# Optimization experiments

Hardware: AMD Instinct MI355X
Metric: run time of the kernel (lower is better)

## Reference

```python
import jax, jax.numpy as jnp
import numpy as np
from jax import lax

B, T, N, CIN, CH, COUT, K, KS, E = 2, 16, 2048, 32, 64, 64, 3, 3, 32768


def setup_inputs() -> dict:
    key = jax.random.key(0)
    ks = jax.random.split(key, 20)
    s = 0.05
    p = lambda k, shp: s * jax.random.normal(k, shp, dtype=jnp.float32)
    return {
        "X": jax.random.normal(ks[0], (B, T, N, CIN), dtype=jnp.float32),
        "edge_index": jax.random.randint(ks[1], (2, E), 0, N),
        "edge_weight": jax.random.uniform(ks[2], (E,), dtype=jnp.float32),
        "tc1_w1": p(ks[3], (CH, CIN, 1, KS)), "tc1_b1": p(ks[4], (CH,)),
        "tc1_w2": p(ks[5], (CH, CIN, 1, KS)), "tc1_b2": p(ks[6], (CH,)),
        "tc1_w3": p(ks[7], (CH, CIN, 1, KS)), "tc1_b3": p(ks[8], (CH,)),
        "cheb_w": p(ks[9], (K, CH, CH)), "cheb_b": p(ks[10], (CH,)),
        "tc2_w1": p(ks[11], (COUT, CH, 1, KS)), "tc2_b1": p(ks[12], (COUT,)),
        "tc2_w2": p(ks[13], (COUT, CH, 1, KS)), "tc2_b2": p(ks[14], (COUT,)),
        "tc2_w3": p(ks[15], (COUT, CH, 1, KS)), "tc2_b3": p(ks[16], (COUT,)),
        "bn_gamma": jnp.ones((N,), jnp.float32),
        "bn_beta": jnp.zeros((N,), jnp.float32),
    }


def _tconv(X, w1, b1, w2, b2, w3, b3):
    # X: (B, T, N, C) -> (B, C, N, T), gated temporal conv over last axis
    x = jnp.transpose(X, (0, 3, 2, 1))
    dn = ("NCHW", "OIHW", "NCHW")
    c = lambda w, b: lax.conv_general_dilated(x, w, (1, 1), "VALID", dimension_numbers=dn) + b[None, :, None, None]
    out = jax.nn.relu(c(w1, b1) + jax.nn.sigmoid(c(w2, b2)) + c(w3, b3))
    return jnp.transpose(out, (0, 3, 2, 1))


def _cheb(x, edge_index, edge_weight, W, b):
    # ChebConv, sym normalization, lambda_max=2 -> L_hat = -D^{-1/2} A D^{-1/2}
    row, col = edge_index[0], edge_index[1]
    w = jnp.where(row == col, 0.0, edge_weight)  # get_laplacian removes self-loops
    deg = jax.ops.segment_sum(w, row, num_segments=N)
    safe = jnp.where(deg > 0, deg, 1.0)
    dis = jnp.where(deg > 0, lax.rsqrt(safe), 0.0)
    norm = -dis[row] * w * dis[col]  # (E,)

    def prop(z):  # z: (B, T, N, C)
        zm = jnp.moveaxis(z, 2, 0)                      # (N, B, T, C)
        msg = zm[col] * norm[:, None, None, None]       # (E, B, T, C)
        agg = jax.ops.segment_sum(msg, row, num_segments=N)
        return jnp.moveaxis(agg, 0, 2)

    Tx0 = x
    out = jnp.einsum("btnc,co->btno", Tx0, W[0])
    Tx1 = prop(Tx0)
    out = out + jnp.einsum("btnc,co->btno", Tx1, W[1])
    for k in range(2, K):
        Tx2 = 2.0 * prop(Tx1) - Tx0
        out = out + jnp.einsum("btnc,co->btno", Tx2, W[k])
        Tx0, Tx1 = Tx1, Tx2
    return out + b


def reference(X, edge_index, edge_weight, tc1_w1, tc1_b1, tc1_w2, tc1_b2, tc1_w3, tc1_b3,
              cheb_w, cheb_b, tc2_w1, tc2_b1, tc2_w2, tc2_b2, tc2_w3, tc2_b3,
              bn_gamma, bn_beta):
    t1 = _tconv(X, tc1_w1, tc1_b1, tc1_w2, tc1_b2, tc1_w3, tc1_b3)   # (B, T-2, N, CH)
    t2 = jax.nn.relu(_cheb(t1, edge_index, edge_weight, cheb_w, cheb_b))
    t3 = _tconv(t2, tc2_w1, tc2_b1, tc2_w2, tc2_b2, tc2_w3, tc2_b3)  # (B, T-4, N, COUT)
    t = jnp.transpose(t3, (0, 2, 1, 3))  # (B, N, T', COUT): N is BN channel axis
    mu = jnp.mean(t, axis=(0, 2, 3), keepdims=True)
    var = jnp.var(t, axis=(0, 2, 3), keepdims=True)
    t = (t - mu) * lax.rsqrt(var + 1e-5) * bn_gamma[None, :, None, None] + bn_beta[None, :, None, None]
    return jnp.transpose(t, (0, 2, 1, 3))
```

## Files before the change

### kernel.cpp

```cpp
#include <hip/hip_runtime.h>
#include <cstdint>
#include <cstddef>

typedef unsigned short ushort_t;
typedef short bf16x8 __attribute__((ext_vector_type(8)));
typedef unsigned short u16x8 __attribute__((ext_vector_type(8)));
typedef float f32x4 __attribute__((ext_vector_type(4)));

#define N_NODES 2048
#define E_EDGES 32768
#define BKT_CAP 64

constexpr int SMALL_TOTAL = 72128;
constexpr int OFS_T1B1 = 6144;
constexpr int OFS_T1B2 = 12352;
constexpr int OFS_T1B3 = 18560;
constexpr int OFS_CHB  = 30912;
constexpr int OFS_T2B1 = 43264;
constexpr int OFS_T2B2 = 55616;
constexpr int OFS_T2B3 = 67968;
constexpr int OFS_GAM  = 68032;
constexpr int OFS_BET  = 70080;

__device__ __align__(16) ushort_t g_t1b [3670016];
__device__ __align__(16) ushort_t g_tx1b[3670016];
__device__ __align__(16) ushort_t g_t2b [3670016];
__device__ __align__(16) float    g_t3 [3145728];
__device__ float    g_deg[N_NODES];
__device__ int      g_cnt[N_NODES];
__device__ int      g_cur[N_NODES];
__device__ __align__(8) int2 g_bkt[N_NODES * BKT_CAP];
__device__ __align__(16) ushort_t g_can[SMALL_TOTAL];
__device__ __align__(16) ushort_t g_wb1[18432];
__device__ __align__(16) ushort_t g_wb2[36864];
__device__ __align__(16) ushort_t g_wbc[12288];

__device__ __forceinline__ float bfu(ushort_t u) { return __uint_as_float(((unsigned)u) << 16); }
__device__ __forceinline__ ushort_t f2bf(float f) {
    unsigned u = __float_as_uint(f);
    u = u + 0x7fffu + ((u >> 16) & 1u);
    return (ushort_t)(u >> 16);
}
__device__ __forceinline__ float ldin(const void* p, int i, bool isbf) {
    return isbf ? bfu(((const ushort_t*)p)[i]) : ((const float*)p)[i];
}
#define BF16_ONES_PAIR 0x3F803F80u

struct SmallPtrs { const void* p[16]; };
struct WPtrs { const void* p[7]; };

__global__ __launch_bounds__(256) void setup_kernel(const int* __restrict__ ei,
                                                    const void* __restrict__ ew,
                                                    SmallPtrs sp, WPtrs wp,
                                                    const unsigned* __restrict__ gam) {
    const bool isbf = (gam[0] == BF16_ONES_PAIR);
    const int blk = blockIdx.x;
    const int tid = threadIdx.x;
    if (blk < 128) {
        int e = blk * 256 + tid;
        int r = ei[e];
        int c = ei[E_EDGES + e];
        float w = (r == c) ? 0.f : ldin(ew, e, isbf);
        atomicAdd(&g_deg[r], w);
        atomicAdd(&g_cnt[r], 1);
        return;
    }
    if (blk < 410) {
        const int sizes[16] = {6144, 64, 6144, 64, 6144, 64, 12288, 64,
                               12288, 64, 12288, 64, 12288, 64, 2048, 2048};
        int idx = (blk - 128) * 256 + tid;
        if (idx >= SMALL_TOTAL) return;
        int j = 0, local = idx;
        while (local >= sizes[j]) { local -= sizes[j]; ++j; }
        g_can[idx] = isbf ? ((const ushort_t*)sp.p[j])[local]
                          : f2bf(((const float*)sp.p[j])[local]);
        return;
    }
    int idx = (blk - 410) * 256 + tid;
    if (idx < 18432) {
        int j = idx & 7, lane = (idx >> 3) & 63, kk = (idx >> 9) % 3;
        int nt = (idx / 1536) & 3, set = idx / 6144;
        int o = nt * 16 + (lane & 15);
        int k = kk * 32 + (lane >> 4) * 8 + j;
        int ci = k & 31, ks = k >> 5;
        g_wb1[idx] = f2bf(ldin(wp.p[set], o * 96 + ci * 3 + ks, isbf));
    } else if (idx < 18432 + 36864) {
        int t = idx - 18432;
        int j = t & 7, lane = (t >> 3) & 63, kk = (t >> 9) % 6;
        int nt = (t / 3072) & 3, set = t / 12288;
        int o = nt * 16 + (lane & 15);
        int k = kk * 32 + (lane >> 4) * 8 + j;
        int ci = k & 63, ks = k >> 6;
        g_wb2[t] = f2bf(ldin(wp.p[3 + set], o * 192 + ci * 3 + ks, isbf));
    } else {
        int t = idx - 18432 - 36864;
        int j = t & 7, lane = (t >> 3) & 63, kk = (t >> 9) % 6;
        int nt = t / 3072;
        int o = nt * 16 + (lane & 15);
        int k = kk * 32 + (lane >> 4) * 8 + j;
        int sec = k >> 6, c = k & 63;
        g_wbc[t] = f2bf(ldin(wp.p[6], sec * 4096 + c * 64 + o, isbf));
    }
}

template <int LAYER>
__global__ __launch_bounds__(256) void tconv_mfma_kernel(const void* __restrict__ Xraw,
                                                         const int* __restrict__ ei,
                                                         const void* __restrict__ ew,
                                                         const unsigned* __restrict__ gam) {
    constexpr int T_in  = (LAYER == 1) ? 16 : 14;
    constexpr int T_out = (LAYER == 1) ? 14 : 12;
    constexpr int KST   = (LAYER == 1) ? 3 : 6;
    constexpr int PADK  = (LAYER == 1) ? 104 : 200;
    constexpr int OB1 = (LAYER == 1) ? OFS_T1B1 : OFS_T2B1;
    constexpr int OB2 = (LAYER == 1) ? OFS_T1B2 : OFS_T2B2;
    constexpr int OB3 = (LAYER == 1) ? OFS_T1B3 : OFS_T2B3;

    const bool isbf = (gam[0] == BF16_ONES_PAIR);

    if constexpr (LAYER == 1) {
        if (blockIdx.x >= 896) {
            int e = (blockIdx.x - 896) * 256 + threadIdx.x;
            int r = ei[e];
            int c = ei[E_EDGES + e];
            float w = (r == c) ? 0.f : ldin(ew, e, isbf);
            float dr = g_deg[r], dc = g_deg[c];
            float nr = dr > 0.f ? rsqrtf(dr) : 0.f;
            float nc = dc > 0.f ? rsqrtf(dc) : 0.f;
            int pos = atomicAdd(&g_cur[r], 1);
            g_bkt[(r << 6) + pos] = make_int2(c, __float_as_int(-nr * w * nc));
            return;
        }
    }

    __shared__ __align__(16) ushort_t xs[64 * PADK];

    const int tid = threadIdx.x;
    const int lane = tid & 63;
    const int wv = tid >> 6;
    const int m0 = blockIdx.x * 64;
    const int n0 = m0 & (N_NODES - 1);
    const int s  = m0 >> 11;
    const int b  = s / T_out;
    const int t  = s - b * T_out;

#pragma unroll
    for (int ks = 0; ks < 3; ++ks) {
        if constexpr (LAYER == 1) {
            const size_t elo = ((size_t)(b * T_in + t + ks) * N_NODES + n0) * 32;
            if (isbf) {
                const ushort4* src = (const ushort4*)((const ushort_t*)Xraw + elo);
                for (int i = tid; i < 512; i += 256) {
                    ushort4 v = src[i];
                    int row = i >> 3, c4 = i & 7;
                    *(ushort4*)&xs[row * PADK + ks * 32 + c4 * 4] = v;
                }
            } else {
                const float4* src = (const float4*)((const float*)Xraw + elo);
                for (int i = tid; i < 512; i += 256) {
                    float4 f = src[i];
                    ushort4 v;
                    v.x = f2bf(f.x); v.y = f2bf(f.y); v.z = f2bf(f.z); v.w = f2bf(f.w);
                    int row = i >> 3, c4 = i & 7;
                    *(ushort4*)&xs[row * PADK + ks * 32 + c4 * 4] = v;
                }
            }
        } else {
            const ushort4* src = (const ushort4*)(g_t2b +
                ((size_t)(b * T_in + t + ks) * N_NODES + n0) * 64);
            for (int i = tid; i < 1024; i += 256) {
                ushort4 v = src[i];
                int row = i >> 4, c4 = i & 15;
                *(ushort4*)&xs[row * PADK + ks * 64 + c4 * 4] = v;
            }
        }
    }
    __syncthreads();

    const ushort_t* WB = (LAYER == 1) ? g_wb1 : g_wb2;
    f32x4 acc[3][4];
#pragma unroll
    for (int st = 0; st < 3; ++st)
#pragma unroll
        for (int nt = 0; nt < 4; ++nt) acc[st][nt] = (f32x4){0.f, 0.f, 0.f, 0.f};

    const int arow = wv * 16 + (lane & 15);
    const int kofs = (lane >> 4) * 8;
#pragma unroll
    for (int kk = 0; kk < KST; ++kk) {
        bf16x8 av = *(const bf16x8*)&xs[arow * PADK + kk * 32 + kofs];
#pragma unroll
        for (int st = 0; st < 3; ++st)
#pragma unroll
            for (int nt = 0; nt < 4; ++nt) {
                bf16x8 bv = ((const bf16x8*)WB)[((st * 4 + nt) * KST + kk) * 64 + lane];
                acc[st][nt] = __builtin_amdgcn_mfma_f32_16x16x32_bf16(av, bv, acc[st][nt], 0, 0, 0);
            }
    }

    const int col = lane & 15;
    const int quad = lane >> 4;
#pragma unroll
    for (int nt = 0; nt < 4; ++nt) {
        int o = nt * 16 + col;
        float b1 = bfu(g_can[OB1 + o]);
        float b2 = bfu(g_can[OB2 + o]);
        float b3 = bfu(g_can[OB3 + o]);
#pragma unroll
        for (int reg = 0; reg < 4; ++reg) {
            int m = m0 + wv * 16 + quad * 4 + reg;
            float q = acc[1][nt][reg] + b2;
            float v = (acc[0][nt][reg] + b1) + 1.f / (1.f + expf(-q)) + (acc[2][nt][reg] + b3);
            v = v > 0.f ? v : 0.f;
            if constexpr (LAYER == 1) g_t1b[(size_t)m * 64 + o] = f2bf(v);
            else                      g_t3 [(size_t)m * 64 + o] = v;
        }
    }
}

__global__ __launch_bounds__(256) void prop0_kernel() {
    const int n = blockIdx.x;
    const int tid = threadIdx.x;
    const int slice = tid >> 3;
    const int ch8   = (tid & 7) * 8;
    if (slice >= 28) return;

    const int beg = n << 6;
    const int end = beg + g_cnt[n];
    const size_t soff = (size_t)slice * (N_NODES * 64) + ch8;

    float a[8];
#pragma unroll
    for (int k = 0; k < 8; ++k) a[k] = 0.f;

    int e = beg;
    for (; e + 4 <= end; e += 4) {
        int2 p0 = g_bkt[e];
        int2 p1 = g_bkt[e + 1];
        int2 p2 = g_bkt[e + 2];
        int2 p3 = g_bkt[e + 3];
        float w0 = __int_as_float(p0.y);
        float w1 = __int_as_float(p1.y);
        float w2 = __int_as_float(p2.y);
        float w3 = __int_as_float(p3.y);
        u16x8 v0 = *(const u16x8*)&g_t1b[soff + ((size_t)p0.x << 6)];
        u16x8 v1 = *(const u16x8*)&g_t1b[soff + ((size_t)p1.x << 6)];
        u16x8 v2 = *(const u16x8*)&g_t1b[soff + ((size_t)p2.x << 6)];
        u16x8 v3 = *(const u16x8*)&g_t1b[soff + ((size_t)p3.x << 6)];
#pragma unroll
        for (int k = 0; k < 8; ++k)
            a[k] = fmaf(w0, bfu(v0[k]), fmaf(w1, bfu(v1[k]),
                   fmaf(w2, bfu(v2[k]), fmaf(w3, bfu(v3[k]), a[k]))));
    }
    for (; e < end; ++e) {
        int2 p = g_bkt[e];
        float w = __int_as_float(p.y);
        u16x8 v = *(const u16x8*)&g_t1b[soff + ((size_t)p.x << 6)];
#pragma unroll
        for (int k = 0; k < 8; ++k) a[k] = fmaf(w, bfu(v[k]), a[k]);
    }

    const size_t o = soff + ((size_t)n << 6);
    u16x8 r;
#pragma unroll
    for (int k = 0; k < 8; ++k) r[k] = f2bf(a[k]);
    *(u16x8*)&g_tx1b[o] = r;
}

__global__ __launch_bounds__(256) void prop_cheb_kernel() {
    __shared__ __align__(16) ushort_t xs[32 * 200];

    const int n = blockIdx.x;
    const int tid = threadIdx.x;
    const int slice = tid >> 3;
    const int ch8   = (tid & 7) * 8;

    if (slice < 28) {
        const int beg = n << 6;
        const int end = beg + g_cnt[n];
        const size_t soff = (size_t)slice * (N_NODES * 64) + ch8;

        float a[8];
#pragma unroll
        for (int k = 0; k < 8; ++k) a[k] = 0.f;

        int e = beg;
        for (; e + 4 <= end; e += 4) {
            int2 p0 = g_bkt[e];
            int2 p1 = g_bkt[e + 1];
            int2 p2 = g_bkt[e + 2];
            int2 p3 = g_bkt[e + 3];
            float w0 = __int_as_float(p0.y);
            float w1 = __int_as_float(p1.y);
            float w2 = __int_as_float(p2.y);
            float w3 = __int_as_float(p3.y);
            u16x8 v0 = *(const u16x8*)&g_tx1b[soff + ((size_t)p0.x << 6)];
            u16x8 v1 = *(const u16x8*)&g_tx1b[soff + ((size_t)p1.x << 6)];
            u16x8 v2 = *(const u16x8*)&g_tx1b[soff + ((size_t)p2.x << 6)];
            u16x8 v3 = *(const u16x8*)&g_tx1b[soff + ((size_t)p3.x << 6)];
#pragma unroll
            for (int k = 0; k < 8; ++k)
                a[k] = fmaf(w0, bfu(v0[k]), fmaf(w1, bfu(v1[k]),
                       fmaf(w2, bfu(v2[k]), fmaf(w3, bfu(v3[k]), a[k]))));
        }
        for (; e < end; ++e) {
            int2 p = g_bkt[e];
            float w = __int_as_float(p.y);
            u16x8 v = *(const u16x8*)&g_tx1b[soff + ((size_t)p.x << 6)];
#pragma unroll
            for (int k = 0; k < 8; ++k) a[k] = fmaf(w, bfu(v[k]), a[k]);
        }

        const size_t o = soff + ((size_t)n << 6);
        u16x8 t0 = *(const u16x8*)&g_t1b[o];
        u16x8 t1 = *(const u16x8*)&g_tx1b[o];
        u16x8 t2;
#pragma unroll
        for (int k = 0; k < 8; ++k) t2[k] = f2bf(2.f * a[k] - bfu(t0[k]));

        *(u16x8*)&xs[slice * 200 + ch8]        = t0;
        *(u16x8*)&xs[slice * 200 + 64 + ch8]   = t1;
        *(u16x8*)&xs[slice * 200 + 128 + ch8]  = t2;
    } else {
        int r = 28 + ((tid - 224) >> 3);
        u16x8 z = {0, 0, 0, 0, 0, 0, 0, 0};
        *(u16x8*)&xs[r * 200 + ch8]       = z;
        *(u16x8*)&xs[r * 200 + 64 + ch8]  = z;
        *(u16x8*)&xs[r * 200 + 128 + ch8] = z;
    }
    __syncthreads();

    const int lane = tid & 63;
    const int wv = tid >> 6;
    const int mt = wv >> 1;
    const int ntb = (wv & 1) * 2;
    const int arow = mt * 16 + (lane & 15);
    const int kofs = (lane >> 4) * 8;

    f32x4 acc[2];
    acc[0] = (f32x4){0.f, 0.f, 0.f, 0.f};
    acc[1] = (f32x4){0.f, 0.f, 0.f, 0.f};
#pragma unroll
    for (int kk = 0; kk < 6; ++kk) {
        bf16x8 av = *(const bf16x8*)&xs[arow * 200 + kk * 32 + kofs];
#pragma unroll
        for (int i = 0; i < 2; ++i) {
            bf16x8 bv = ((const bf16x8*)g_wbc)[((ntb + i) * 6 + kk) * 64 + lane];
            acc[i] = __builtin_amdgcn_mfma_f32_16x16x32_bf16(av, bv, acc[i], 0, 0, 0);
        }
    }

    const int col = lane & 15;
    const int quad = lane >> 4;
#pragma unroll
    for (int i = 0; i < 2; ++i) {
        int o = (ntb + i) * 16 + col;
        float bias = bfu(g_can[OFS_CHB + o]);
#pragma unroll
        for (int reg = 0; reg < 4; ++reg) {
            int m = mt * 16 + quad * 4 + reg;
            if (m < 28) {
                float v = acc[i][reg] + bias;
                g_t2b[((size_t)(m * N_NODES + n)) * 64 + o] = f2bf(v > 0.f ? v : 0.f);
            }
        }
    }
}

__global__ __launch_bounds__(256) void bn_fused_kernel(void* __restrict__ outp,
                                                       const unsigned* __restrict__ gam) {
    int n = blockIdx.x;
    int tid = threadIdx.x;

    if (n < 8) {
        int z = n * 256 + tid;
        g_deg[z] = 0.f; g_cnt[z] = 0; g_cur[z] = 0;
    }

    int q = tid & 15;
    int g = tid >> 4;
    const bool two = (g < 8);

    size_t base0 = ((size_t)(g * N_NODES + n)) * 64 + q * 4;
    float4 v0 = *reinterpret_cast<const float4*>(&g_t3[base0]);
    float s1 = v0.x + v0.y + v0.z + v0.w;
    float s2 = v0.x * v0.x + v0.y * v0.y + v0.z * v0.z + v0.w * v0.w;
    size_t base1 = 0;
    float4 v1 = make_float4(0.f, 0.f, 0.f, 0.f);
    if (two) {
        base1 = ((size_t)((g + 16) * N_NODES + n)) * 64 + q * 4;
        v1 = *reinterpret_cast<const float4*>(&g_t3[base1]);
        s1 += v1.x + v1.y + v1.z + v1.w;
        s2 += v1.x * v1.x + v1.y * v1.y + v1.z * v1.z + v1.w * v1.w;
    }

    __shared__ float r1[256], r2[256];
    __shared__ float sc_s, sh_s;
    r1[tid] = s1;
    r2[tid] = s2;
    __syncthreads();
    for (int st = 128; st > 0; st >>= 1) {
        if (tid < st) { r1[tid] += r1[tid + st]; r2[tid] += r2[tid + st]; }
        __syncthreads();
    }
    if (tid == 0) {
        const float inv = 1.f / 1536.f;
        float mean = r1[0] * inv;
        float var  = r2[0] * inv - mean * mean;
        float rstd = rsqrtf(var + 1e-5f);
        float gm = bfu(g_can[OFS_GAM + n]), be = bfu(g_can[OFS_BET + n]);
        sc_s = rstd * gm;
        sh_s = be - mean * rstd * gm;
    }
    __syncthreads();
    float sc = sc_s, sh = sh_s;
    bool isbf = (gam[0] == BF16_ONES_PAIR);

    if (isbf) {
        ushort4 o0;
        o0.x = f2bf(v0.x * sc + sh); o0.y = f2bf(v0.y * sc + sh);
        o0.z = f2bf(v0.z * sc + sh); o0.w = f2bf(v0.w * sc + sh);
        *reinterpret_cast<ushort4*>((ushort_t*)outp + base0) = o0;
        if (two) {
            ushort4 o1;
            o1.x = f2bf(v1.x * sc + sh); o1.y = f2bf(v1.y * sc + sh);
            o1.z = f2bf(v1.z * sc + sh); o1.w = f2bf(v1.w * sc + sh);
            *reinterpret_cast<ushort4*>((ushort_t*)outp + base1) = o1;
        }
    } else {
        float4 o0 = make_float4(v0.x * sc + sh, v0.y * sc + sh, v0.z * sc + sh, v0.w * sc + sh);
        *reinterpret_cast<float4*>((float*)outp + base0) = o0;
        if (two) {
            float4 o1 = make_float4(v1.x * sc + sh, v1.y * sc + sh, v1.z * sc + sh, v1.w * sc + sh);
            *reinterpret_cast<float4*>((float*)outp + base1) = o1;
        }
    }
}

extern "C" void kernel_launch(void* const* d_in, const int* in_sizes, int n_in,
                              void* d_out, int out_size, void* d_ws, size_t ws_size,
                              hipStream_t stream) {
    const void* X = d_in[0];
    const int* ei = (const int*)d_in[1];
    const void* ew = d_in[2];
    const unsigned* gam = (const unsigned*)d_in[17];

    SmallPtrs sp;
    for (int i = 0; i < 16; ++i) sp.p[i] = d_in[3 + i];
    WPtrs wp;
    wp.p[0] = d_in[3];  wp.p[1] = d_in[5];  wp.p[2] = d_in[7];
    wp.p[3] = d_in[11]; wp.p[4] = d_in[13]; wp.p[5] = d_in[15];
    wp.p[6] = d_in[9];

    setup_kernel<<<674, 256, 0, stream>>>(ei, ew, sp, wp, gam);
    tconv_mfma_kernel<1><<<1024, 256, 0, stream>>>(X, ei, ew, gam);
    prop0_kernel<<<N_NODES, 256, 0, stream>>>();
    prop_cheb_kernel<<<N_NODES, 256, 0, stream>>>();
    tconv_mfma_kernel<2><<<768, 256, 0, stream>>>(X, nullptr, nullptr, gam);
    bn_fused_kernel<<<N_NODES, 256, 0, stream>>>(d_out, gam);
}
```

Measured before the change: 164.9 us.

## Fuse Chebyshev projection, second temporal conv and batchnorm into one per-node kernel

Merges the cheb output projection, the second gated temporal convolution and the per-node batch norm into one kernel with one block per node. The relu'd cheb output stays in shared memory and feeds the tconv2 MFMA directly, and the batch-norm statistics are reduced from registers. This removes the g_t2b and g_t3 global round trips and two kernel launches. In exchange the per-node blocks do small MFMA tiles with padded rows, and the scratch-counter reset moves to the end of the fused kernel.

```diff
diff --git a/kernel.cpp b/kernel.cpp
--- a/kernel.cpp
+++ b/kernel.cpp
@@ -24,8 +24,6 @@
 
 __device__ __align__(16) ushort_t g_t1b [3670016];
 __device__ __align__(16) ushort_t g_tx1b[3670016];
-__device__ __align__(16) ushort_t g_t2b [3670016];
-__device__ __align__(16) float    g_t3 [3145728];
 __device__ float    g_deg[N_NODES];
 __device__ int      g_cnt[N_NODES];
 __device__ int      g_cur[N_NODES];
@@ -103,34 +101,28 @@
     }
 }
 
-template <int LAYER>
-__global__ __launch_bounds__(256) void tconv_mfma_kernel(const void* __restrict__ Xraw,
-                                                         const int* __restrict__ ei,
-                                                         const void* __restrict__ ew,
-                                                         const unsigned* __restrict__ gam) {
-    constexpr int T_in  = (LAYER == 1) ? 16 : 14;
-    constexpr int T_out = (LAYER == 1) ? 14 : 12;
-    constexpr int KST   = (LAYER == 1) ? 3 : 6;
-    constexpr int PADK  = (LAYER == 1) ? 104 : 200;
-    constexpr int OB1 = (LAYER == 1) ? OFS_T1B1 : OFS_T2B1;
-    constexpr int OB2 = (LAYER == 1) ? OFS_T1B2 : OFS_T2B2;
-    constexpr int OB3 = (LAYER == 1) ? OFS_T1B3 : OFS_T2B3;
+__global__ __launch_bounds__(256) void tconv1_mfma_kernel(const void* __restrict__ Xraw,
+                                                          const int* __restrict__ ei,
+                                                          const void* __restrict__ ew,
+                                                          const unsigned* __restrict__ gam) {
+    constexpr int T_in  = 16;
+    constexpr int T_out = 14;
+    constexpr int KST   = 3;
+    constexpr int PADK  = 104;
 
     const bool isbf = (gam[0] == BF16_ONES_PAIR);
 
-    if constexpr (LAYER == 1) {
-        if (blockIdx.x >= 896) {
-            int e = (blockIdx.x - 896) * 256 + threadIdx.x;
-            int r = ei[e];
-            int c = ei[E_EDGES + e];
-            float w = (r == c) ? 0.f : ldin(ew, e, isbf);
-            float dr = g_deg[r], dc = g_deg[c];
-            float nr = dr > 0.f ? rsqrtf(dr) : 0.f;
-            float nc = dc > 0.f ? rsqrtf(dc) : 0.f;
-            int pos = atomicAdd(&g_cur[r], 1);
-            g_bkt[(r << 6) + pos] = make_int2(c, __float_as_int(-nr * w * nc));
-            return;
-        }
+    if (blockIdx.x >= 896) {
+        int e = (blockIdx.x - 896) * 256 + threadIdx.x;
+        int r = ei[e];
+        int c = ei[E_EDGES + e];
+        float w = (r == c) ? 0.f : ldin(ew, e, isbf);
+        float dr = g_deg[r], dc = g_deg[c];
+        float nr = dr > 0.f ? rsqrtf(dr) : 0.f;
+        float nc = dc > 0.f ? rsqrtf(dc) : 0.f;
+        int pos = atomicAdd(&g_cur[r], 1);
+        g_bkt[(r << 6) + pos] = make_int2(c, __float_as_int(-nr * w * nc));
+        return;
     }
 
     __shared__ __align__(16) ushort_t xs[64 * PADK];
@@ -146,38 +138,27 @@
 
 #pragma unroll
     for (int ks = 0; ks < 3; ++ks) {
-        if constexpr (LAYER == 1) {
-            const size_t elo = ((size_t)(b * T_in + t + ks) * N_NODES + n0) * 32;
-            if (isbf) {
-                const ushort4* src = (const ushort4*)((const ushort_t*)Xraw + elo);
-                for (int i = tid; i < 512; i += 256) {
-                    ushort4 v = src[i];
-                    int row = i >> 3, c4 = i & 7;
-                    *(ushort4*)&xs[row * PADK + ks * 32 + c4 * 4] = v;
-                }
-            } else {
-                const float4* src = (const float4*)((const float*)Xraw + elo);
-                for (int i = tid; i < 512; i += 256) {
-                    float4 f = src[i];
-                    ushort4 v;
-                    v.x = f2bf(f.x); v.y = f2bf(f.y); v.z = f2bf(f.z); v.w = f2bf(f.w);
-                    int row = i >> 3, c4 = i & 7;
-                    *(ushort4*)&xs[row * PADK + ks * 32 + c4 * 4] = v;
-                }
+        const size_t elo = ((size_t)(b * T_in + t + ks) * N_NODES + n0) * 32;
+        if (isbf) {
+            const ushort4* src = (const ushort4*)((const ushort_t*)Xraw + elo);
+            for (int i = tid; i < 512; i += 256) {
+                ushort4 v = src[i];
+                int row = i >> 3, c4 = i & 7;
+                *(ushort4*)&xs[row * PADK + ks * 32 + c4 * 4] = v;
             }
         } else {
-            const ushort4* src = (const ushort4*)(g_t2b +
-                ((size_t)(b * T_in + t + ks) * N_NODES + n0) * 64);
-            for (int i = tid; i < 1024; i += 256) {
-                ushort4 v = src[i];
-                int row = i >> 4, c4 = i & 15;
-                *(ushort4*)&xs[row * PADK + ks * 64 + c4 * 4] = v;
+            const float4* src = (const float4*)((const float*)Xraw + elo);
+            for (int i = tid; i < 512; i += 256) {
+                float4 f = src[i];
+                ushort4 v;
+                v.x = f2bf(f.x); v.y = f2bf(f.y); v.z = f2bf(f.z); v.w = f2bf(f.w);
+                int row = i >> 3, c4 = i & 7;
+                *(ushort4*)&xs[row * PADK + ks * 32 + c4 * 4] = v;
             }
         }
     }
     __syncthreads();
 
-    const ushort_t* WB = (LAYER == 1) ? g_wb1 : g_wb2;
     f32x4 acc[3][4];
 #pragma unroll
     for (int st = 0; st < 3; ++st)
@@ -193,7 +174,7 @@
         for (int st = 0; st < 3; ++st)
 #pragma unroll
             for (int nt = 0; nt < 4; ++nt) {
-                bf16x8 bv = ((const bf16x8*)WB)[((st * 4 + nt) * KST + kk) * 64 + lane];
+                bf16x8 bv = ((const bf16x8*)g_wb1)[((st * 4 + nt) * KST + kk) * 64 + lane];
                 acc[st][nt] = __builtin_amdgcn_mfma_f32_16x16x32_bf16(av, bv, acc[st][nt], 0, 0, 0);
             }
     }
@@ -203,17 +184,16 @@
 #pragma unroll
     for (int nt = 0; nt < 4; ++nt) {
         int o = nt * 16 + col;
-        float b1 = bfu(g_can[OB1 + o]);
-        float b2 = bfu(g_can[OB2 + o]);
-        float b3 = bfu(g_can[OB3 + o]);
+        float b1 = bfu(g_can[OFS_T1B1 + o]);
+        float b2 = bfu(g_can[OFS_T1B2 + o]);
+        float b3 = bfu(g_can[OFS_T1B3 + o]);
 #pragma unroll
         for (int reg = 0; reg < 4; ++reg) {
             int m = m0 + wv * 16 + quad * 4 + reg;
             float q = acc[1][nt][reg] + b2;
             float v = (acc[0][nt][reg] + b1) + 1.f / (1.f + expf(-q)) + (acc[2][nt][reg] + b3);
             v = v > 0.f ? v : 0.f;
-            if constexpr (LAYER == 1) g_t1b[(size_t)m * 64 + o] = f2bf(v);
-            else                      g_t3 [(size_t)m * 64 + o] = v;
+            g_t1b[(size_t)m * 64 + o] = f2bf(v);
         }
     }
 }
@@ -267,8 +247,12 @@
     *(u16x8*)&g_tx1b[o] = r;
 }
 
-__global__ __launch_bounds__(256) void prop_cheb_kernel() {
+__global__ __launch_bounds__(256) void fused_tail_kernel(void* __restrict__ outp,
+                                                         const unsigned* __restrict__ gam) {
     __shared__ __align__(16) ushort_t xs[32 * 200];
+    __shared__ __align__(16) ushort_t t2s[28 * 72];
+    __shared__ float r1[256], r2[256];
+    __shared__ float sc_s, sh_s;
 
     const int n = blockIdx.x;
     const int tid = threadIdx.x;
@@ -334,68 +318,83 @@
     const int wv = tid >> 6;
     const int mt = wv >> 1;
     const int ntb = (wv & 1) * 2;
-    const int arow = mt * 16 + (lane & 15);
-    const int kofs = (lane >> 4) * 8;
-
-    f32x4 acc[2];
-    acc[0] = (f32x4){0.f, 0.f, 0.f, 0.f};
-    acc[1] = (f32x4){0.f, 0.f, 0.f, 0.f};
-#pragma unroll
-    for (int kk = 0; kk < 6; ++kk) {
-        bf16x8 av = *(const bf16x8*)&xs[arow * 200 + kk * 32 + kofs];
-#pragma unroll
-        for (int i = 0; i < 2; ++i) {
-            bf16x8 bv = ((const bf16x8*)g_wbc)[((ntb + i) * 6 + kk) * 64 + lane];
-            acc[i] = __builtin_amdgcn_mfma_f32_16x16x32_bf16(av, bv, acc[i], 0, 0, 0);
-        }
-    }
-
     const int col = lane & 15;
     const int quad = lane >> 4;
+    const int arow = mt * 16 + col;
+    const int kofs = quad * 8;
+
+    {
+        f32x4 accb[2];
+        accb[0] = (f32x4){0.f, 0.f, 0.f, 0.f};
+        accb[1] = (f32x4){0.f, 0.f, 0.f, 0.f};
+#pragma unroll
+        for (int kk = 0; kk < 6; ++kk) {
+            bf16x8 av = *(const bf16x8*)&xs[arow * 200 + kk * 32 + kofs];
+#pragma unroll
+            for (int i = 0; i < 2; ++i) {
+                bf16x8 bv = ((const bf16x8*)g_wbc)[((ntb + i) * 6 + kk) * 64 + lane];
+                accb[i] = __builtin_amdgcn_mfma_f32_16x16x32_bf16(av, bv, accb[i], 0, 0, 0);
+            }
+        }
+#pragma unroll
+        for (int i = 0; i < 2; ++i) {
+            int o = (ntb + i) * 16 + col;
+            float bias = bfu(g_can[OFS_CHB + o]);
+#pragma unroll
+            for (int reg = 0; reg < 4; ++reg) {
+                int s = mt * 16 + quad * 4 + reg;
+                if (s < 28) {
+                    float v = accb[i][reg] + bias;
+                    t2s[s * 72 + o] = f2bf(v > 0.f ? v : 0.f);
+                }
+            }
+        }
+    }
+    __syncthreads();
+
+    const int m_a = arow;
+    const int bb  = (m_a >= 12) ? 1 : 0;
+    const int rbase = (m_a < 24) ? (m_a + 2 * bb) : 0;
+
+    f32x4 acc2[3][2];
+#pragma unroll
+    for (int st = 0; st < 3; ++st)
+#pragma unroll
+        for (int i = 0; i < 2; ++i) acc2[st][i] = (f32x4){0.f, 0.f, 0.f, 0.f};
+
+#pragma unroll
+    for (int kk = 0; kk < 6; ++kk) {
+        const int ks = kk >> 1;
+        const int ci0 = (kk & 1) * 32;
+        bf16x8 av = *(const bf16x8*)&t2s[(rbase + ks) * 72 + ci0 + kofs];
+#pragma unroll
+        for (int st = 0; st < 3; ++st)
+#pragma unroll
+            for (int i = 0; i < 2; ++i) {
+                bf16x8 bv = ((const bf16x8*)g_wb2)[((st * 4 + ntb + i) * 6 + kk) * 64 + lane];
+                acc2[st][i] = __builtin_amdgcn_mfma_f32_16x16x32_bf16(av, bv, acc2[st][i], 0, 0, 0);
+            }
+    }
+
+    float y[2][4];
+    float s1 = 0.f, s2 = 0.f;
 #pragma unroll
     for (int i = 0; i < 2; ++i) {
         int o = (ntb + i) * 16 + col;
-        float bias = bfu(g_can[OFS_CHB + o]);
+        float b1 = bfu(g_can[OFS_T2B1 + o]);
+        float b2 = bfu(g_can[OFS_T2B2 + o]);
+        float b3 = bfu(g_can[OFS_T2B3 + o]);
 #pragma unroll
         for (int reg = 0; reg < 4; ++reg) {
-            int m = mt * 16 + quad * 4 + reg;
-            if (m < 28) {
-                float v = acc[i][reg] + bias;
-                g_t2b[((size_t)(m * N_NODES + n)) * 64 + o] = f2bf(v > 0.f ? v : 0.f);
-            }
-        }
-    }
-}
-
-__global__ __launch_bounds__(256) void bn_fused_kernel(void* __restrict__ outp,
-                                                       const unsigned* __restrict__ gam) {
-    int n = blockIdx.x;
-    int tid = threadIdx.x;
-
-    if (n < 8) {
-        int z = n * 256 + tid;
-        g_deg[z] = 0.f; g_cnt[z] = 0; g_cur[z] = 0;
-    }
-
-    int q = tid & 15;
-    int g = tid >> 4;
-    const bool two = (g < 8);
-
-    size_t base0 = ((size_t)(g * N_NODES + n)) * 64 + q * 4;
-    float4 v0 = *reinterpret_cast<const float4*>(&g_t3[base0]);
-    float s1 = v0.x + v0.y + v0.z + v0.w;
-    float s2 = v0.x * v0.x + v0.y * v0.y + v0.z * v0.z + v0.w * v0.w;
-    size_t base1 = 0;
-    float4 v1 = make_float4(0.f, 0.f, 0.f, 0.f);
-    if (two) {
-        base1 = ((size_t)((g + 16) * N_NODES + n)) * 64 + q * 4;
-        v1 = *reinterpret_cast<const float4*>(&g_t3[base1]);
-        s1 += v1.x + v1.y + v1.z + v1.w;
-        s2 += v1.x * v1.x + v1.y * v1.y + v1.z * v1.z + v1.w * v1.w;
-    }
-
-    __shared__ float r1[256], r2[256];
-    __shared__ float sc_s, sh_s;
+            int mm = mt * 16 + quad * 4 + reg;
+            float q = acc2[1][i][reg] + b2;
+            float v = (acc2[0][i][reg] + b1) + 1.f / (1.f + expf(-q)) + (acc2[2][i][reg] + b3);
+            v = v > 0.f ? v : 0.f;
+            y[i][reg] = v;
+            if (mm < 24) { s1 += v; s2 += v * v; }
+        }
+    }
+
     r1[tid] = s1;
     r2[tid] = s2;
     __syncthreads();
@@ -413,28 +412,25 @@
         sh_s = be - mean * rstd * gm;
     }
     __syncthreads();
-    float sc = sc_s, sh = sh_s;
-    bool isbf = (gam[0] == BF16_ONES_PAIR);
-
-    if (isbf) {
-        ushort4 o0;
-        o0.x = f2bf(v0.x * sc + sh); o0.y = f2bf(v0.y * sc + sh);
-        o0.z = f2bf(v0.z * sc + sh); o0.w = f2bf(v0.w * sc + sh);
-        *reinterpret_cast<ushort4*>((ushort_t*)outp + base0) = o0;
-        if (two) {
-            ushort4 o1;
-            o1.x = f2bf(v1.x * sc + sh); o1.y = f2bf(v1.y * sc + sh);
-            o1.z = f2bf(v1.z * sc + sh); o1.w = f2bf(v1.w * sc + sh);
-            *reinterpret_cast<ushort4*>((ushort_t*)outp + base1) = o1;
-        }
-    } else {
-        float4 o0 = make_float4(v0.x * sc + sh, v0.y * sc + sh, v0.z * sc + sh, v0.w * sc + sh);
-        *reinterpret_cast<float4*>((float*)outp + base0) = o0;
-        if (two) {
-            float4 o1 = make_float4(v1.x * sc + sh, v1.y * sc + sh, v1.z * sc + sh, v1.w * sc + sh);
-            *reinterpret_cast<float4*>((float*)outp + base1) = o1;
-        }
-    }
+    const float sc = sc_s, sh = sh_s;
+    const bool isbf = (gam[0] == BF16_ONES_PAIR);
+
+#pragma unroll
+    for (int i = 0; i < 2; ++i) {
+        int o = (ntb + i) * 16 + col;
+#pragma unroll
+        for (int reg = 0; reg < 4; ++reg) {
+            int mm = mt * 16 + quad * 4 + reg;
+            if (mm < 24) {
+                size_t off = ((size_t)mm * N_NODES + n) * 64 + o;
+                float yy = y[i][reg] * sc + sh;
+                if (isbf) ((ushort_t*)outp)[off] = f2bf(yy);
+                else      ((float*)outp)[off] = yy;
+            }
+        }
+    }
+
+    if (tid == 0) { g_deg[n] = 0.f; g_cnt[n] = 0; g_cur[n] = 0; }
 }
 
 extern "C" void kernel_launch(void* const* d_in, const int* in_sizes, int n_in,
@@ -453,9 +449,7 @@
     wp.p[6] = d_in[9];
 
     setup_kernel<<<674, 256, 0, stream>>>(ei, ew, sp, wp, gam);
-    tconv_mfma_kernel<1><<<1024, 256, 0, stream>>>(X, ei, ew, gam);
+    tconv1_mfma_kernel<<<1024, 256, 0, stream>>>(X, ei, ew, gam);
     prop0_kernel<<<N_NODES, 256, 0, stream>>>();
-    prop_cheb_kernel<<<N_NODES, 256, 0, stream>>>();
-    tconv_mfma_kernel<2><<<768, 256, 0, stream>>>(X, nullptr, nullptr, gam);
-    bn_fused_kernel<<<N_NODES, 256, 0, stream>>>(d_out, gam);
-}
+    fused_tail_kernel<<<N_NODES, 256, 0, stream>>>(d_out, gam);
+}
```

Result: slower. 171.9 us (+4.2%).

## Bucket edges in setup pass and apply symmetric normalization lazily in propagation

Applied to the files above, without the earlier changes.

Edge bucketing now happens during the degree pass in the setup kernel, storing raw weights rather than normalized ones. The separate edge-pass blocks in the first temporal conv are replaced by a small pass that converts degrees to inverse square roots in place. The propagation kernels then rebuild each edge's norm on the fly from the stored weight and the two D^-1/2 values. This removes one full pass over the edge list and its atomics, at the cost of an extra gathered g_deg load and two multiplies per edge in both propagation kernels. The templated tconv kernel is also split into two specialised kernels.

```diff
diff --git a/kernel.cpp b/kernel.cpp
--- a/kernel.cpp
+++ b/kernel.cpp
@@ -27,7 +27,6 @@
 __device__ __align__(16) ushort_t g_t2b [3670016];
 __device__ __align__(16) float    g_t3 [3145728];
 __device__ float    g_deg[N_NODES];
-__device__ int      g_cnt[N_NODES];
 __device__ int      g_cur[N_NODES];
 __device__ __align__(8) int2 g_bkt[N_NODES * BKT_CAP];
 __device__ __align__(16) ushort_t g_can[SMALL_TOTAL];
@@ -62,7 +61,8 @@
         int c = ei[E_EDGES + e];
         float w = (r == c) ? 0.f : ldin(ew, e, isbf);
         atomicAdd(&g_deg[r], w);
-        atomicAdd(&g_cnt[r], 1);
+        int pos = atomicAdd(&g_cur[r], 1);
+        g_bkt[(r << 6) + pos] = make_int2(c, __float_as_int(w));
         return;
     }
     if (blk < 410) {
@@ -103,34 +103,20 @@
     }
 }
 
-template <int LAYER>
-__global__ __launch_bounds__(256) void tconv_mfma_kernel(const void* __restrict__ Xraw,
-                                                         const int* __restrict__ ei,
-                                                         const void* __restrict__ ew,
-                                                         const unsigned* __restrict__ gam) {
-    constexpr int T_in  = (LAYER == 1) ? 16 : 14;
-    constexpr int T_out = (LAYER == 1) ? 14 : 12;
-    constexpr int KST   = (LAYER == 1) ? 3 : 6;
-    constexpr int PADK  = (LAYER == 1) ? 104 : 200;
-    constexpr int OB1 = (LAYER == 1) ? OFS_T1B1 : OFS_T2B1;
-    constexpr int OB2 = (LAYER == 1) ? OFS_T1B2 : OFS_T2B2;
-    constexpr int OB3 = (LAYER == 1) ? OFS_T1B3 : OFS_T2B3;
+__global__ __launch_bounds__(256) void tconv1_mfma_kernel(const void* __restrict__ Xraw,
+                                                          const unsigned* __restrict__ gam) {
+    constexpr int T_in  = 16;
+    constexpr int T_out = 14;
+    constexpr int KST   = 3;
+    constexpr int PADK  = 104;
 
     const bool isbf = (gam[0] == BF16_ONES_PAIR);
 
-    if constexpr (LAYER == 1) {
-        if (blockIdx.x >= 896) {
-            int e = (blockIdx.x - 896) * 256 + threadIdx.x;
-            int r = ei[e];
-            int c = ei[E_EDGES + e];
-            float w = (r == c) ? 0.f : ldin(ew, e, isbf);
-            float dr = g_deg[r], dc = g_deg[c];
-            float nr = dr > 0.f ? rsqrtf(dr) : 0.f;
-            float nc = dc > 0.f ? rsqrtf(dc) : 0.f;
-            int pos = atomicAdd(&g_cur[r], 1);
-            g_bkt[(r << 6) + pos] = make_int2(c, __float_as_int(-nr * w * nc));
-            return;
-        }
+    if (blockIdx.x >= 896) {
+        int z = (blockIdx.x - 896) * 256 + threadIdx.x;
+        float d = g_deg[z];
+        g_deg[z] = d > 0.f ? rsqrtf(d) : 0.f;
+        return;
     }
 
     __shared__ __align__(16) ushort_t xs[64 * PADK];
@@ -146,38 +132,27 @@
 
 #pragma unroll
     for (int ks = 0; ks < 3; ++ks) {
-        if constexpr (LAYER == 1) {
-            const size_t elo = ((size_t)(b * T_in + t + ks) * N_NODES + n0) * 32;
-            if (isbf) {
-                const ushort4* src = (const ushort4*)((const ushort_t*)Xraw + elo);
-                for (int i = tid; i < 512; i += 256) {
-                    ushort4 v = src[i];
-                    int row = i >> 3, c4 = i & 7;
-                    *(ushort4*)&xs[row * PADK + ks * 32 + c4 * 4] = v;
-                }
-            } else {
-                const float4* src = (const float4*)((const float*)Xraw + elo);
-                for (int i = tid; i < 512; i += 256) {
-                    float4 f = src[i];
-                    ushort4 v;
-                    v.x = f2bf(f.x); v.y = f2bf(f.y); v.z = f2bf(f.z); v.w = f2bf(f.w);
-                    int row = i >> 3, c4 = i & 7;
-                    *(ushort4*)&xs[row * PADK + ks * 32 + c4 * 4] = v;
-                }
+        const size_t elo = ((size_t)(b * T_in + t + ks) * N_NODES + n0) * 32;
+        if (isbf) {
+            const ushort4* src = (const ushort4*)((const ushort_t*)Xraw + elo);
+            for (int i = tid; i < 512; i += 256) {
+                ushort4 v = src[i];
+                int row = i >> 3, c4 = i & 7;
+                *(ushort4*)&xs[row * PADK + ks * 32 + c4 * 4] = v;
             }
         } else {
-            const ushort4* src = (const ushort4*)(g_t2b +
-                ((size_t)(b * T_in + t + ks) * N_NODES + n0) * 64);
-            for (int i = tid; i < 1024; i += 256) {
-                ushort4 v = src[i];
-                int row = i >> 4, c4 = i & 15;
-                *(ushort4*)&xs[row * PADK + ks * 64 + c4 * 4] = v;
+            const float4* src = (const float4*)((const float*)Xraw + elo);
+            for (int i = tid; i < 512; i += 256) {
+                float4 f = src[i];
+                ushort4 v;
+                v.x = f2bf(f.x); v.y = f2bf(f.y); v.z = f2bf(f.z); v.w = f2bf(f.w);
+                int row = i >> 3, c4 = i & 7;
+                *(ushort4*)&xs[row * PADK + ks * 32 + c4 * 4] = v;
             }
         }
     }
     __syncthreads();
 
-    const ushort_t* WB = (LAYER == 1) ? g_wb1 : g_wb2;
     f32x4 acc[3][4];
 #pragma unroll
     for (int st = 0; st < 3; ++st)
@@ -193,7 +168,7 @@
         for (int st = 0; st < 3; ++st)
 #pragma unroll
             for (int nt = 0; nt < 4; ++nt) {
-                bf16x8 bv = ((const bf16x8*)WB)[((st * 4 + nt) * KST + kk) * 64 + lane];
+                bf16x8 bv = ((const bf16x8*)g_wb1)[((st * 4 + nt) * KST + kk) * 64 + lane];
                 acc[st][nt] = __builtin_amdgcn_mfma_f32_16x16x32_bf16(av, bv, acc[st][nt], 0, 0, 0);
             }
     }
@@ -203,17 +178,16 @@
 #pragma unroll
     for (int nt = 0; nt < 4; ++nt) {
         int o = nt * 16 + col;
-        float b1 = bfu(g_can[OB1 + o]);
-        float b2 = bfu(g_can[OB2 + o]);
-        float b3 = bfu(g_can[OB3 + o]);
+        float b1 = bfu(g_can[OFS_T1B1 + o]);
+        float b2 = bfu(g_can[OFS_T1B2 + o]);
+        float b3 = bfu(g_can[OFS_T1B3 + o]);
 #pragma unroll
         for (int reg = 0; reg < 4; ++reg) {
             int m = m0 + wv * 16 + quad * 4 + reg;
             float q = acc[1][nt][reg] + b2;
             float v = (acc[0][nt][reg] + b1) + 1.f / (1.f + expf(-q)) + (acc[2][nt][reg] + b3);
             v = v > 0.f ? v : 0.f;
-            if constexpr (LAYER == 1) g_t1b[(size_t)m * 64 + o] = f2bf(v);
-            else                      g_t3 [(size_t)m * 64 + o] = v;
+            g_t1b[(size_t)m * 64 + o] = f2bf(v);
         }
     }
 }
@@ -226,7 +200,8 @@
     if (slice >= 28) return;
 
     const int beg = n << 6;
-    const int end = beg + g_cnt[n];
+    const int end = beg + g_cur[n];
+    const float nr = g_deg[n];
     const size_t soff = (size_t)slice * (N_NODES * 64) + ch8;
 
     float a[8];
@@ -239,10 +214,10 @@
         int2 p1 = g_bkt[e + 1];
         int2 p2 = g_bkt[e + 2];
         int2 p3 = g_bkt[e + 3];
-        float w0 = __int_as_float(p0.y);
-        float w1 = __int_as_float(p1.y);
-        float w2 = __int_as_float(p2.y);
-        float w3 = __int_as_float(p3.y);
+        float w0 = -nr * __int_as_float(p0.y) * g_deg[p0.x];
+        float w1 = -nr * __int_as_float(p1.y) * g_deg[p1.x];
+        float w2 = -nr * __int_as_float(p2.y) * g_deg[p2.x];
+        float w3 = -nr * __int_as_float(p3.y) * g_deg[p3.x];
         u16x8 v0 = *(const u16x8*)&g_t1b[soff + ((size_t)p0.x << 6)];
         u16x8 v1 = *(const u16x8*)&g_t1b[soff + ((size_t)p1.x << 6)];
         u16x8 v2 = *(const u16x8*)&g_t1b[soff + ((size_t)p2.x << 6)];
@@ -254,7 +229,7 @@
     }
     for (; e < end; ++e) {
         int2 p = g_bkt[e];
-        float w = __int_as_float(p.y);
+        float w = -nr * __int_as_float(p.y) * g_deg[p.x];
         u16x8 v = *(const u16x8*)&g_t1b[soff + ((size_t)p.x << 6)];
 #pragma unroll
         for (int k = 0; k < 8; ++k) a[k] = fmaf(w, bfu(v[k]), a[k]);
@@ -277,7 +252,8 @@
 
     if (slice < 28) {
         const int beg = n << 6;
-        const int end = beg + g_cnt[n];
+        const int end = beg + g_cur[n];
+        const float nr = g_deg[n];
         const size_t soff = (size_t)slice * (N_NODES * 64) + ch8;
 
         float a[8];
@@ -290,10 +266,10 @@
             int2 p1 = g_bkt[e + 1];
             int2 p2 = g_bkt[e + 2];
             int2 p3 = g_bkt[e + 3];
-            float w0 = __int_as_float(p0.y);
-            float w1 = __int_as_float(p1.y);
-            float w2 = __int_as_float(p2.y);
-            float w3 = __int_as_float(p3.y);
+            float w0 = -nr * __int_as_float(p0.y) * g_deg[p0.x];
+            float w1 = -nr * __int_as_float(p1.y) * g_deg[p1.x];
+            float w2 = -nr * __int_as_float(p2.y) * g_deg[p2.x];
+            float w3 = -nr * __int_as_float(p3.y) * g_deg[p3.x];
             u16x8 v0 = *(const u16x8*)&g_tx1b[soff + ((size_t)p0.x << 6)];
             u16x8 v1 = *(const u16x8*)&g_tx1b[soff + ((size_t)p1.x << 6)];
             u16x8 v2 = *(const u16x8*)&g_tx1b[soff + ((size_t)p2.x << 6)];
@@ -305,7 +281,7 @@
         }
         for (; e < end; ++e) {
             int2 p = g_bkt[e];
-            float w = __int_as_float(p.y);
+            float w = -nr * __int_as_float(p.y) * g_deg[p.x];
             u16x8 v = *(const u16x8*)&g_tx1b[soff + ((size_t)p.x << 6)];
 #pragma unroll
             for (int k = 0; k < 8; ++k) a[k] = fmaf(w, bfu(v[k]), a[k]);
@@ -367,6 +343,74 @@
     }
 }
 
+__global__ __launch_bounds__(256) void tconv2_mfma_kernel() {
+    constexpr int T_in  = 14;
+    constexpr int T_out = 12;
+    constexpr int KST   = 6;
+    constexpr int PADK  = 200;
+
+    __shared__ __align__(16) ushort_t xs[64 * PADK];
+
+    const int tid = threadIdx.x;
+    const int lane = tid & 63;
+    const int wv = tid >> 6;
+    const int m0 = blockIdx.x * 64;
+    const int n0 = m0 & (N_NODES - 1);
+    const int s  = m0 >> 11;
+    const int b  = s / T_out;
+    const int t  = s - b * T_out;
+
+#pragma unroll
+    for (int ks = 0; ks < 3; ++ks) {
+        const ushort4* src = (const ushort4*)(g_t2b +
+            ((size_t)(b * T_in + t + ks) * N_NODES + n0) * 64);
+        for (int i = tid; i < 1024; i += 256) {
+            ushort4 v = src[i];
+            int row = i >> 4, c4 = i & 15;
+            *(ushort4*)&xs[row * PADK + ks * 64 + c4 * 4] = v;
+        }
+    }
+    __syncthreads();
+
+    f32x4 acc[3][4];
+#pragma unroll
+    for (int st = 0; st < 3; ++st)
+#pragma unroll
+        for (int nt = 0; nt < 4; ++nt) acc[st][nt] = (f32x4){0.f, 0.f, 0.f, 0.f};
+
+    const int arow = wv * 16 + (lane & 15);
+    const int kofs = (lane >> 4) * 8;
+#pragma unroll
+    for (int kk = 0; kk < KST; ++kk) {
+        bf16x8 av = *(const bf16x8*)&xs[arow * PADK + kk * 32 + kofs];
+#pragma unroll
+        for (int st = 0; st < 3; ++st)
+#pragma unroll
+            for (int nt = 0; nt < 4; ++nt) {
+                bf16x8 bv = ((const bf16x8*)g_wb2)[((st * 4 + nt) * KST + kk) * 64 + lane];
+                acc[st][nt] = __builtin_amdgcn_mfma_f32_16x16x32_bf16(av, bv, acc[st][nt], 0, 0, 0);
+            }
+    }
+
+    const int col = lane & 15;
+    const int quad = lane >> 4;
+#pragma unroll
+    for (int nt = 0; nt < 4; ++nt) {
+        int o = nt * 16 + col;
+        float b1 = bfu(g_can[OFS_T2B1 + o]);
+        float b2 = bfu(g_can[OFS_T2B2 + o]);
+        float b3 = bfu(g_can[OFS_T2B3 + o]);
+#pragma unroll
+        for (int reg = 0; reg < 4; ++reg) {
+            int m = m0 + wv * 16 + quad * 4 + reg;
+            float q = acc[1][nt][reg] + b2;
+            float v = (acc[0][nt][reg] + b1) + 1.f / (1.f + expf(-q)) + (acc[2][nt][reg] + b3);
+            v = v > 0.f ? v : 0.f;
+            g_t3[(size_t)m * 64 + o] = v;
+        }
+    }
+}
+
 __global__ __launch_bounds__(256) void bn_fused_kernel(void* __restrict__ outp,
                                                        const unsigned* __restrict__ gam) {
     int n = blockIdx.x;
@@ -374,7 +418,7 @@
 
     if (n < 8) {
         int z = n * 256 + tid;
-        g_deg[z] = 0.f; g_cnt[z] = 0; g_cur[z] = 0;
+        g_deg[z] = 0.f; g_cur[z] = 0;
     }
 
     int q = tid & 15;
@@ -453,9 +497,9 @@
     wp.p[6] = d_in[9];
 
     setup_kernel<<<674, 256, 0, stream>>>(ei, ew, sp, wp, gam);
-    tconv_mfma_kernel<1><<<1024, 256, 0, stream>>>(X, ei, ew, gam);
+    tconv1_mfma_kernel<<<904, 256, 0, stream>>>(X, gam);
     prop0_kernel<<<N_NODES, 256, 0, stream>>>();
     prop_cheb_kernel<<<N_NODES, 256, 0, stream>>>();
-    tconv_mfma_kernel<2><<<768, 256, 0, stream>>>(X, nullptr, nullptr, gam);
+    tconv2_mfma_kernel<<<768, 256, 0, stream>>>();
     bn_fused_kernel<<<N_NODES, 256, 0, stream>>>(d_out, gam);
 }
```

Result: slower. 182.2 us (+10.5%).
